# Kernel optimization log

Measured on AMD Instinct MI355X. Metric: run time of the kernel, lower is better.

The kernel has to match this reference:

```python
import jax, jax.numpy as jnp
import numpy as np

B, L, T = 8, 4096, 128
D_H, D_G, D_PROJ = 1024, 256, 256


def setup_inputs() -> dict:
    key = jax.random.key(0)
    k1, k2, k3, k4, k5 = jax.random.split(key, 5)
    H = jax.random.normal(k1, (B, L, D_H), dtype=jnp.float32)
    G = jax.random.normal(k2, (B, T, D_G), dtype=jnp.float32)
    mask = jax.random.randint(k3, (B, L), 0, 2) == 1  # True = masked out
    Wk = jax.random.normal(k4, (D_H, D_PROJ), dtype=jnp.float32) * 0.02
    Wq = jax.random.normal(k5, (D_G, D_PROJ), dtype=jnp.float32) * 0.02
    return {"H": H, "G": G, "mask": mask, "Wk": Wk, "Wq": Wq}


def reference(H, G, mask, Wk, Wq):
    scale = D_PROJ ** (-0.5)
    K = jnp.einsum('bld,dp->blp', H, Wk)          # [B, L, d_proj]
    Q = jnp.einsum('btd,dp->btp', G, Wq)          # [B, T, d_proj]
    logits = jnp.einsum('btp,blp->btl', Q, K) * scale  # [B, T, L]
    logits = jnp.where(mask[:, None, :], -jnp.inf, logits)
    alpha = jax.nn.softmax(logits, axis=-1)       # [B, T, L]
    Z = jnp.einsum('btl,bld->btd', alpha, H)      # [B, T, d_h]
    return Z
```

## Files before the change

kernel.cpp:

```cpp
#include <hip/hip_runtime.h>
#include <hip/hip_bf16.h>
#include <math.h>

#define B_  8
#define L_  4096
#define T_  128
#define DH  1024
#define DG  256
#define DP  256
#define BK  64
#define ZCH 8

typedef short bf16x8 __attribute__((ext_vector_type(8)));
typedef float f32x4  __attribute__((ext_vector_type(4)));
typedef unsigned short u16x8 __attribute__((ext_vector_type(8)));

#define AS1(p) ((const __attribute__((address_space(1))) void*)(p))
#define AS3(p) ((__attribute__((address_space(3))) void*)(p))

__device__ __forceinline__ unsigned short f2bf(float f) {
    unsigned u = __float_as_uint(f);
    unsigned r = (u + 0x7FFFu + ((u >> 16) & 1u)) >> 16;
    return (unsigned short)r;
}

__global__ __launch_bounds__(256) void wct_kernel(const float* __restrict__ Wk,
                                                  const float* __restrict__ Wq,
                                                  unsigned short* __restrict__ Wct) {
    __shared__ __attribute__((aligned(16))) unsigned short As[128 * BK];
    __shared__ __attribute__((aligned(16))) unsigned short Bs[64 * BK];
    const int n0 = blockIdx.x * 64, m0 = blockIdx.y * 128;
    const int tid = threadIdx.x, wave = tid >> 6, lane = tid & 63;
    const int lm = lane & 15, quad = lane >> 4;
    const int wm = wave >> 1, wn = wave & 1;
    const int bc = (tid & 15) * 4, br = tid >> 4;
    f32x4 acc[4][2] = {};

    for (int k0 = 0; k0 < DP; k0 += BK) {
        #pragma unroll
        for (int s = 0; s < 8; ++s) {
            const int row = br + s * 16;
            const float4 v = *(const float4*)(Wk + (size_t)(m0 + row) * DP + k0 + bc);
            ushort4 p; p.x = f2bf(v.x); p.y = f2bf(v.y); p.z = f2bf(v.z); p.w = f2bf(v.w);
            *(ushort4*)(&As[row * BK + bc]) = p;
        }
        #pragma unroll
        for (int s = 0; s < 4; ++s) {
            const int row = br + s * 16;
            const float4 v = *(const float4*)(Wq + (size_t)(n0 + row) * DP + k0 + bc);
            ushort4 p; p.x = f2bf(v.x); p.y = f2bf(v.y); p.z = f2bf(v.z); p.w = f2bf(v.w);
            *(ushort4*)(&Bs[row * BK + bc]) = p;
        }
        __syncthreads();
        #pragma unroll
        for (int ks = 0; ks < 2; ++ks) {
            bf16x8 a[4], bf[2];
            #pragma unroll
            for (int i = 0; i < 4; ++i)
                a[i] = *(const bf16x8*)(&As[(wm * 64 + i * 16 + lm) * BK + ks * 32 + quad * 8]);
            #pragma unroll
            for (int j = 0; j < 2; ++j)
                bf[j] = *(const bf16x8*)(&Bs[(wn * 32 + j * 16 + lm) * BK + ks * 32 + quad * 8]);
            #pragma unroll
            for (int i = 0; i < 4; ++i)
                #pragma unroll
                for (int j = 0; j < 2; ++j)
                    acc[i][j] = __builtin_amdgcn_mfma_f32_16x16x32_bf16(a[i], bf[j], acc[i][j], 0, 0, 0);
        }
        __syncthreads();
    }
    unsigned short* Cb = Wct + (size_t)m0 * DG + n0;
    #pragma unroll
    for (int i = 0; i < 4; ++i)
        #pragma unroll
        for (int j = 0; j < 2; ++j)
            #pragma unroll
            for (int r = 0; r < 4; ++r)
                Cb[(size_t)(wm * 64 + i * 16 + quad * 4 + r) * DG + wn * 32 + j * 16 + lm] =
                    f2bf(acc[i][j][r] * 0.0625f);
}

__global__ __launch_bounds__(256) void qproj_kernel(const float* __restrict__ G,
                                                    const unsigned short* __restrict__ Wct,
                                                    unsigned short* __restrict__ Qk) {
    __shared__ __attribute__((aligned(16))) unsigned short As[128 * BK];
    __shared__ __attribute__((aligned(16))) unsigned short Bs[64 * BK];
    const int n0 = blockIdx.x * 64, m0 = blockIdx.y * 128;
    const int tid = threadIdx.x, wave = tid >> 6, lane = tid & 63;
    const int lm = lane & 15, quad = lane >> 4;
    const int wm = wave >> 1, wn = wave & 1;
    const int bc = (tid & 15) * 4, br = tid >> 4;
    const int ar = lane >> 3, akb = (lane & 7) * 8;
    f32x4 acc[4][2] = {};

    for (int k0 = 0; k0 < DG; k0 += BK) {
        #pragma unroll
        for (int s = 0; s < 8; ++s) {
            const int row = br + s * 16;
            const float4 v = *(const float4*)(G + (size_t)(m0 + row) * DG + k0 + bc);
            ushort4 p; p.x = f2bf(v.x); p.y = f2bf(v.y); p.z = f2bf(v.z); p.w = f2bf(v.w);
            *(ushort4*)(&As[row * BK + bc]) = p;
        }
        #pragma unroll
        for (int s = 0; s < 2; ++s) {
            const int rowb = s * 32 + wave * 8;
            const unsigned short* gp = Wct + (size_t)(n0 + rowb + ar) * DG + k0 + akb;
            __builtin_amdgcn_global_load_lds(AS1(gp), AS3(&Bs[rowb * BK]), 16, 0, 0);
        }
        __syncthreads();
        #pragma unroll
        for (int ks = 0; ks < 2; ++ks) {
            bf16x8 a[4], bf[2];
            #pragma unroll
            for (int i = 0; i < 4; ++i)
                a[i] = *(const bf16x8*)(&As[(wm * 64 + i * 16 + lm) * BK + ks * 32 + quad * 8]);
            #pragma unroll
            for (int j = 0; j < 2; ++j)
                bf[j] = *(const bf16x8*)(&Bs[(wn * 32 + j * 16 + lm) * BK + ks * 32 + quad * 8]);
            #pragma unroll
            for (int i = 0; i < 4; ++i)
                #pragma unroll
                for (int j = 0; j < 2; ++j)
                    acc[i][j] = __builtin_amdgcn_mfma_f32_16x16x32_bf16(a[i], bf[j], acc[i][j], 0, 0, 0);
        }
        __syncthreads();
    }
    unsigned short* Cb = Qk + (size_t)m0 * DH + n0;
    #pragma unroll
    for (int i = 0; i < 4; ++i)
        #pragma unroll
        for (int j = 0; j < 2; ++j)
            #pragma unroll
            for (int r = 0; r < 4; ++r)
                Cb[(size_t)(wm * 64 + i * 16 + quad * 4 + r) * DH + wn * 32 + j * 16 + lm] =
                    f2bf(acc[i][j][r]);
}

__global__ __launch_bounds__(256, 2) void fusedsm_kernel(const unsigned short* __restrict__ Qk,
                                                         const float* __restrict__ H,
                                                         const int* __restrict__ mask,
                                                         unsigned short* __restrict__ alpha,
                                                         float* __restrict__ rowsum,
                                                         unsigned short* __restrict__ H16) {
    __shared__ __attribute__((aligned(16))) unsigned short As[T_ * BK];
    __shared__ __attribute__((aligned(16))) unsigned short Bs[64 * BK];
    __shared__ float rs[T_];
    const int blin = blockIdx.x + (L_ / 64) * blockIdx.y;
    const int b = blin & 7, l0 = (blin >> 3) * 64;
    const int tid = threadIdx.x, wave = tid >> 6, lane = tid & 63;
    const unsigned short* Ab = Qk + (size_t)b * T_ * DH;
    const float*          Hb = H + ((size_t)b * L_ + l0) * DH;
    unsigned short*     H16b = H16 + ((size_t)b * L_ + l0) * DH;

    const int lm = lane & 15, quad = lane >> 4;
    const int wm = wave >> 1, wn = wave & 1;
    f32x4 acc[4][2] = {};
    const int ar = lane >> 3, akb = (lane & 7) * 8;
    const int bc = (tid & 15) * 4, br = tid >> 4;

    if (tid < T_) rs[tid] = 0.f;

    for (int k0 = 0; k0 < DH; k0 += BK) {
        #pragma unroll
        for (int s = 0; s < 4; ++s) {
            const int rowb = s * 32 + wave * 8;
            const unsigned short* gp = Ab + (size_t)(rowb + ar) * DH + k0 + akb;
            __builtin_amdgcn_global_load_lds(AS1(gp), AS3(&As[rowb * BK]), 16, 0, 0);
        }
        #pragma unroll
        for (int s = 0; s < 4; ++s) {
            const int row = br + s * 16;
            const float4 v = *(const float4*)(Hb + (size_t)row * DH + k0 + bc);
            ushort4 pk; pk.x = f2bf(v.x); pk.y = f2bf(v.y); pk.z = f2bf(v.z); pk.w = f2bf(v.w);
            *(ushort4*)(&Bs[row * BK + bc]) = pk;
            *(ushort4*)(H16b + (size_t)row * DH + k0 + bc) = pk;
        }
        __syncthreads();
        #pragma unroll
        for (int ks = 0; ks < 2; ++ks) {
            bf16x8 a[4], bf[2];
            #pragma unroll
            for (int i = 0; i < 4; ++i)
                a[i] = *(const bf16x8*)(&As[(wm * 64 + i * 16 + lm) * BK + ks * 32 + quad * 8]);
            #pragma unroll
            for (int j = 0; j < 2; ++j)
                bf[j] = *(const bf16x8*)(&Bs[(wn * 32 + j * 16 + lm) * BK + ks * 32 + quad * 8]);
            #pragma unroll
            for (int i = 0; i < 4; ++i)
                #pragma unroll
                for (int j = 0; j < 2; ++j)
                    acc[i][j] = __builtin_amdgcn_mfma_f32_16x16x32_bf16(a[i], bf[j], acc[i][j], 0, 0, 0);
        }
        __syncthreads();
    }

    const int c0 = l0 + wn * 32 + lm;
    const int mk0 = mask[(size_t)b * L_ + c0];
    const int mk1 = mask[(size_t)b * L_ + c0 + 16];
    unsigned short* Arow = alpha + (size_t)b * T_ * L_ + l0 + wn * 32 + lm;
    #pragma unroll
    for (int i = 0; i < 4; ++i) {
        #pragma unroll
        for (int r = 0; r < 4; ++r) {
            const int row = wm * 64 + i * 16 + quad * 4 + r;
            float e0 = mk0 ? 0.f : __expf(acc[i][0][r]);
            float e1 = mk1 ? 0.f : __expf(acc[i][1][r]);
            Arow[(size_t)row * L_]      = f2bf(e0);
            Arow[(size_t)row * L_ + 16] = f2bf(e1);
            float part = e0 + e1;
            part += __shfl_xor(part, 1, 64);
            part += __shfl_xor(part, 2, 64);
            part += __shfl_xor(part, 4, 64);
            part += __shfl_xor(part, 8, 64);
            if (lm == 0) atomicAdd(&rs[row], part);
        }
    }
    __syncthreads();
    if (tid < T_) atomicAdd(&rowsum[(size_t)b * T_ + tid], rs[tid]);
}

__global__ __launch_bounds__(256, 2) void z_kernel(const unsigned short* __restrict__ alpha,
                                                   const unsigned short* __restrict__ H16,
                                                   const float* __restrict__ rowsum,
                                                   float* __restrict__ Z) {
    __shared__ __attribute__((aligned(16))) unsigned short As[T_ * BK];
    __shared__ __attribute__((aligned(16))) unsigned B32[128 * 32];
    const int blin = blockIdx.x + 8 * (blockIdx.y + 8 * blockIdx.z);
    const int ch = blin & 7, rest = blin >> 3;
    const int b = rest & 7, d0 = (rest >> 3) * 128;
    const int tid = threadIdx.x, wave = tid >> 6, lane = tid & 63;
    const int Lc = L_ / ZCH;
    const unsigned short* Ab = alpha + (size_t)b * T_ * L_ + ch * Lc;
    const unsigned short* Hb = H16 + ((size_t)b * L_ + ch * Lc) * DH + d0;

    const int lm = lane & 15, quad = lane >> 4;
    const int wm = wave >> 1, wn = wave & 1;
    f32x4 acc[4][4] = {};
    const int ar = lane >> 3, akb = (lane & 7) * 8;
    const int dg = tid & 15, lph = tid >> 4;

    for (int k0 = 0; k0 < Lc; k0 += BK) {
        #pragma unroll
        for (int s = 0; s < 4; ++s) {
            const int rowb = s * 32 + wave * 8;
            const unsigned short* gp = Ab + (size_t)(rowb + ar) * L_ + k0 + akb;
            __builtin_amdgcn_global_load_lds(AS1(gp), AS3(&As[rowb * BK]), 16, 0, 0);
        }
        {
            const unsigned short* r = Hb + (size_t)(k0 + 4 * lph) * DH + dg * 8;
            u16x8 u[4];
            #pragma unroll
            for (int rr = 0; rr < 4; ++rr)
                u[rr] = *(const u16x8*)(r + (size_t)rr * DH);
            const int lp0 = 2 * lph;
            #pragma unroll
            for (int i = 0; i < 8; ++i) {
                const int d   = dg * 8 + i;
                const int rot = ((i + (dg & 7)) << 2) & 31;
                B32[d * 32 + ((lp0 + rot) & 31)] =
                    (unsigned)u[0][i] | ((unsigned)u[1][i] << 16);
                B32[d * 32 + ((lp0 + 1 + rot) & 31)] =
                    (unsigned)u[2][i] | ((unsigned)u[3][i] << 16);
            }
        }
        __syncthreads();
        #pragma unroll
        for (int ks = 0; ks < 2; ++ks) {
            bf16x8 a[4], bf[4];
            #pragma unroll
            for (int i = 0; i < 4; ++i)
                a[i] = *(const bf16x8*)(&As[(wm * 64 + i * 16 + lm) * BK + ks * 32 + quad * 8]);
            #pragma unroll
            for (int j = 0; j < 4; ++j) {
                const int d   = wn * 64 + j * 16 + lm;
                const int rot = (((d & 7) + ((d >> 3) & 7)) << 2) & 31;
                bf[j] = *(const bf16x8*)(&B32[d * 32 + ((ks * 16 + quad * 4 + rot) & 31)]);
            }
            #pragma unroll
            for (int i = 0; i < 4; ++i)
                #pragma unroll
                for (int j = 0; j < 4; ++j)
                    acc[i][j] = __builtin_amdgcn_mfma_f32_16x16x32_bf16(a[i], bf[j], acc[i][j], 0, 0, 0);
        }
        __syncthreads();
    }
    float* Zb = Z + ((size_t)b * T_) * DH + d0;
    const float* rsb = rowsum + (size_t)b * T_;
    #pragma unroll
    for (int i = 0; i < 4; ++i) {
        #pragma unroll
        for (int r = 0; r < 4; ++r) {
            const int row = wm * 64 + i * 16 + quad * 4 + r;
            const float inv = 1.0f / rsb[row];
            #pragma unroll
            for (int j = 0; j < 4; ++j)
                atomicAdd(&Zb[(size_t)row * DH + wn * 64 + j * 16 + lm], acc[i][j][r] * inv);
        }
    }
}

extern "C" void kernel_launch(void* const* d_in, const int* in_sizes, int n_in,
                              void* d_out, int out_size, void* d_ws, size_t ws_size,
                              hipStream_t stream) {
    const float* H    = (const float*)d_in[0];
    const float* G    = (const float*)d_in[1];
    const int*   mask = (const int*)d_in[2];
    const float* Wk   = (const float*)d_in[3];
    const float* Wq   = (const float*)d_in[4];
    float* Z = (float*)d_out;

    char* ws = (char*)d_ws;
    unsigned short* Wct    = (unsigned short*)ws;
    unsigned short* Qk     = (unsigned short*)(ws + ((size_t)1 << 20));
    unsigned short* alpha  = (unsigned short*)(ws + ((size_t)4 << 20));
    float*          rowsum = (float*)(ws + ((size_t)13 << 20));
    unsigned short* H16    = (unsigned short*)(ws + ((size_t)14 << 20));

    hipMemsetAsync(rowsum, 0, (size_t)B_ * T_ * sizeof(float), stream);
    hipMemsetAsync(Z, 0, (size_t)B_ * T_ * DH * sizeof(float), stream);
    wct_kernel<<<dim3(DG / 64, DH / 128), 256, 0, stream>>>(Wk, Wq, Wct);
    qproj_kernel<<<dim3(DH / 64, (B_ * T_) / 128), 256, 0, stream>>>(G, Wct, Qk);
    fusedsm_kernel<<<dim3(L_ / 64, B_), 256, 0, stream>>>(Qk, H, mask, alpha, rowsum, H16);
    z_kernel<<<dim3(DH / 128, B_, ZCH), 256, 0, stream>>>(alpha, H16, rowsum, Z);
}
```

Baseline: 306.5 us.

## Double-buffer LDS in score and Z GEMMs; replace Z atomics with partial reduction

```diff
diff --git a/kernel.cpp b/kernel.cpp
--- a/kernel.cpp
+++ b/kernel.cpp
@@ -142,8 +142,8 @@
                                                          unsigned short* __restrict__ alpha,
                                                          float* __restrict__ rowsum,
                                                          unsigned short* __restrict__ H16) {
-    __shared__ __attribute__((aligned(16))) unsigned short As[T_ * BK];
-    __shared__ __attribute__((aligned(16))) unsigned short Bs[64 * BK];
+    __shared__ __attribute__((aligned(16))) unsigned short As[2][T_ * BK];
+    __shared__ __attribute__((aligned(16))) unsigned short Bs[2][64 * BK];
     __shared__ float rs[T_];
     const int blin = blockIdx.x + (L_ / 64) * blockIdx.y;
     const int b = blin & 7, l0 = (blin >> 3) * 64;
@@ -160,36 +160,66 @@
 
     if (tid < T_) rs[tid] = 0.f;
 
-    for (int k0 = 0; k0 < DH; k0 += BK) {
+    {
         #pragma unroll
         for (int s = 0; s < 4; ++s) {
             const int rowb = s * 32 + wave * 8;
-            const unsigned short* gp = Ab + (size_t)(rowb + ar) * DH + k0 + akb;
-            __builtin_amdgcn_global_load_lds(AS1(gp), AS3(&As[rowb * BK]), 16, 0, 0);
+            const unsigned short* gp = Ab + (size_t)(rowb + ar) * DH + akb;
+            __builtin_amdgcn_global_load_lds(AS1(gp), AS3(&As[0][rowb * BK]), 16, 0, 0);
         }
         #pragma unroll
         for (int s = 0; s < 4; ++s) {
             const int row = br + s * 16;
-            const float4 v = *(const float4*)(Hb + (size_t)row * DH + k0 + bc);
+            const float4 v = *(const float4*)(Hb + (size_t)row * DH + bc);
             ushort4 pk; pk.x = f2bf(v.x); pk.y = f2bf(v.y); pk.z = f2bf(v.z); pk.w = f2bf(v.w);
-            *(ushort4*)(&Bs[row * BK + bc]) = pk;
-            *(ushort4*)(H16b + (size_t)row * DH + k0 + bc) = pk;
-        }
-        __syncthreads();
+            *(ushort4*)(&Bs[0][row * BK + bc]) = pk;
+            *(ushort4*)(H16b + (size_t)row * DH + bc) = pk;
+        }
+    }
+    __syncthreads();
+
+    const int nT = DH / BK;
+    for (int t = 0; t < nT; ++t) {
+        const int p = t & 1, q = p ^ 1;
+        const int k1 = (t + 1) * BK;
+        float4 v[4];
+        if (t + 1 < nT) {
+            #pragma unroll
+            for (int s = 0; s < 4; ++s) {
+                const int rowb = s * 32 + wave * 8;
+                const unsigned short* gp = Ab + (size_t)(rowb + ar) * DH + k1 + akb;
+                __builtin_amdgcn_global_load_lds(AS1(gp), AS3(&As[q][rowb * BK]), 16, 0, 0);
+            }
+            #pragma unroll
+            for (int s = 0; s < 4; ++s) {
+                const int row = br + s * 16;
+                v[s] = *(const float4*)(Hb + (size_t)row * DH + k1 + bc);
+            }
+        }
         #pragma unroll
         for (int ks = 0; ks < 2; ++ks) {
             bf16x8 a[4], bf[2];
             #pragma unroll
             for (int i = 0; i < 4; ++i)
-                a[i] = *(const bf16x8*)(&As[(wm * 64 + i * 16 + lm) * BK + ks * 32 + quad * 8]);
+                a[i] = *(const bf16x8*)(&As[p][(wm * 64 + i * 16 + lm) * BK + ks * 32 + quad * 8]);
             #pragma unroll
             for (int j = 0; j < 2; ++j)
-                bf[j] = *(const bf16x8*)(&Bs[(wn * 32 + j * 16 + lm) * BK + ks * 32 + quad * 8]);
+                bf[j] = *(const bf16x8*)(&Bs[p][(wn * 32 + j * 16 + lm) * BK + ks * 32 + quad * 8]);
             #pragma unroll
             for (int i = 0; i < 4; ++i)
                 #pragma unroll
                 for (int j = 0; j < 2; ++j)
                     acc[i][j] = __builtin_amdgcn_mfma_f32_16x16x32_bf16(a[i], bf[j], acc[i][j], 0, 0, 0);
+        }
+        if (t + 1 < nT) {
+            #pragma unroll
+            for (int s = 0; s < 4; ++s) {
+                const int row = br + s * 16;
+                ushort4 pk; pk.x = f2bf(v[s].x); pk.y = f2bf(v[s].y);
+                pk.z = f2bf(v[s].z); pk.w = f2bf(v[s].w);
+                *(ushort4*)(&Bs[q][row * BK + bc]) = pk;
+                *(ushort4*)(H16b + (size_t)row * DH + k1 + bc) = pk;
+            }
         }
         __syncthreads();
     }
@@ -221,10 +251,9 @@
 
 __global__ __launch_bounds__(256, 2) void z_kernel(const unsigned short* __restrict__ alpha,
                                                    const unsigned short* __restrict__ H16,
-                                                   const float* __restrict__ rowsum,
-                                                   float* __restrict__ Z) {
-    __shared__ __attribute__((aligned(16))) unsigned short As[T_ * BK];
-    __shared__ __attribute__((aligned(16))) unsigned B32[128 * 32];
+                                                   float* __restrict__ part) {
+    __shared__ __attribute__((aligned(16))) unsigned short As[2][T_ * BK];
+    __shared__ __attribute__((aligned(16))) unsigned B32[2][128 * 32];
     const int blin = blockIdx.x + 8 * (blockIdx.y + 8 * blockIdx.z);
     const int ch = blin & 7, rest = blin >> 3;
     const int b = rest & 7, d0 = (rest >> 3) * 128;
@@ -238,65 +267,101 @@
     f32x4 acc[4][4] = {};
     const int ar = lane >> 3, akb = (lane & 7) * 8;
     const int dg = tid & 15, lph = tid >> 4;
-
-    for (int k0 = 0; k0 < Lc; k0 += BK) {
+    const int lp0 = 2 * lph;
+
+    {
         #pragma unroll
         for (int s = 0; s < 4; ++s) {
             const int rowb = s * 32 + wave * 8;
-            const unsigned short* gp = Ab + (size_t)(rowb + ar) * L_ + k0 + akb;
-            __builtin_amdgcn_global_load_lds(AS1(gp), AS3(&As[rowb * BK]), 16, 0, 0);
-        }
-        {
-            const unsigned short* r = Hb + (size_t)(k0 + 4 * lph) * DH + dg * 8;
-            u16x8 u[4];
+            const unsigned short* gp = Ab + (size_t)(rowb + ar) * L_ + akb;
+            __builtin_amdgcn_global_load_lds(AS1(gp), AS3(&As[0][rowb * BK]), 16, 0, 0);
+        }
+        const unsigned short* r = Hb + (size_t)(4 * lph) * DH + dg * 8;
+        u16x8 u[4];
+        #pragma unroll
+        for (int rr = 0; rr < 4; ++rr)
+            u[rr] = *(const u16x8*)(r + (size_t)rr * DH);
+        #pragma unroll
+        for (int i = 0; i < 8; ++i) {
+            const int d   = dg * 8 + i;
+            const int rot = ((i + (dg & 7)) << 2) & 31;
+            B32[0][d * 32 + ((lp0 + rot) & 31)]     = (unsigned)u[0][i] | ((unsigned)u[1][i] << 16);
+            B32[0][d * 32 + ((lp0 + 1 + rot) & 31)] = (unsigned)u[2][i] | ((unsigned)u[3][i] << 16);
+        }
+    }
+    __syncthreads();
+
+    const int nT = Lc / BK;
+    for (int t = 0; t < nT; ++t) {
+        const int p = t & 1, q = p ^ 1;
+        const int k1 = (t + 1) * BK;
+        u16x8 u[4];
+        if (t + 1 < nT) {
+            #pragma unroll
+            for (int s = 0; s < 4; ++s) {
+                const int rowb = s * 32 + wave * 8;
+                const unsigned short* gp = Ab + (size_t)(rowb + ar) * L_ + k1 + akb;
+                __builtin_amdgcn_global_load_lds(AS1(gp), AS3(&As[q][rowb * BK]), 16, 0, 0);
+            }
+            const unsigned short* r = Hb + (size_t)(k1 + 4 * lph) * DH + dg * 8;
             #pragma unroll
             for (int rr = 0; rr < 4; ++rr)
                 u[rr] = *(const u16x8*)(r + (size_t)rr * DH);
-            const int lp0 = 2 * lph;
+        }
+        #pragma unroll
+        for (int ks = 0; ks < 2; ++ks) {
+            bf16x8 a[4], bf[4];
+            #pragma unroll
+            for (int i = 0; i < 4; ++i)
+                a[i] = *(const bf16x8*)(&As[p][(wm * 64 + i * 16 + lm) * BK + ks * 32 + quad * 8]);
+            #pragma unroll
+            for (int j = 0; j < 4; ++j) {
+                const int d   = wn * 64 + j * 16 + lm;
+                const int rot = (((d & 7) + ((d >> 3) & 7)) << 2) & 31;
+                bf[j] = *(const bf16x8*)(&B32[p][d * 32 + ((ks * 16 + quad * 4 + rot) & 31)]);
+            }
+            #pragma unroll
+            for (int i = 0; i < 4; ++i)
+                #pragma unroll
+                for (int j = 0; j < 4; ++j)
+                    acc[i][j] = __builtin_amdgcn_mfma_f32_16x16x32_bf16(a[i], bf[j], acc[i][j], 0, 0, 0);
+        }
+        if (t + 1 < nT) {
             #pragma unroll
             for (int i = 0; i < 8; ++i) {
                 const int d   = dg * 8 + i;
                 const int rot = ((i + (dg & 7)) << 2) & 31;
-                B32[d * 32 + ((lp0 + rot) & 31)] =
-                    (unsigned)u[0][i] | ((unsigned)u[1][i] << 16);
-                B32[d * 32 + ((lp0 + 1 + rot) & 31)] =
-                    (unsigned)u[2][i] | ((unsigned)u[3][i] << 16);
-            }
-        }
-        __syncthreads();
-        #pragma unroll
-        for (int ks = 0; ks < 2; ++ks) {
-            bf16x8 a[4], bf[4];
-            #pragma unroll
-            for (int i = 0; i < 4; ++i)
-                a[i] = *(const bf16x8*)(&As[(wm * 64 + i * 16 + lm) * BK + ks * 32 + quad * 8]);
-            #pragma unroll
-            for (int j = 0; j < 4; ++j) {
-                const int d   = wn * 64 + j * 16 + lm;
-                const int rot = (((d & 7) + ((d >> 3) & 7)) << 2) & 31;
-                bf[j] = *(const bf16x8*)(&B32[d * 32 + ((ks * 16 + quad * 4 + rot) & 31)]);
-            }
-            #pragma unroll
-            for (int i = 0; i < 4; ++i)
-                #pragma unroll
-                for (int j = 0; j < 4; ++j)
-                    acc[i][j] = __builtin_amdgcn_mfma_f32_16x16x32_bf16(a[i], bf[j], acc[i][j], 0, 0, 0);
-        }
-        __syncthreads();
-    }
-    float* Zb = Z + ((size_t)b * T_) * DH + d0;
-    const float* rsb = rowsum + (size_t)b * T_;
-    #pragma unroll
-    for (int i = 0; i < 4; ++i) {
-        #pragma unroll
-        for (int r = 0; r < 4; ++r) {
-            const int row = wm * 64 + i * 16 + quad * 4 + r;
-            const float inv = 1.0f / rsb[row];
-            #pragma unroll
-            for (int j = 0; j < 4; ++j)
-                atomicAdd(&Zb[(size_t)row * DH + wn * 64 + j * 16 + lm], acc[i][j][r] * inv);
-        }
-    }
+                B32[q][d * 32 + ((lp0 + rot) & 31)]     = (unsigned)u[0][i] | ((unsigned)u[1][i] << 16);
+                B32[q][d * 32 + ((lp0 + 1 + rot) & 31)] = (unsigned)u[2][i] | ((unsigned)u[3][i] << 16);
+            }
+        }
+        __syncthreads();
+    }
+    float* Cb = part + (((size_t)ch * B_ + b) * T_) * DH + d0;
+    #pragma unroll
+    for (int i = 0; i < 4; ++i)
+        #pragma unroll
+        for (int j = 0; j < 4; ++j)
+            #pragma unroll
+            for (int r = 0; r < 4; ++r)
+                Cb[(size_t)(wm * 64 + i * 16 + quad * 4 + r) * DH + wn * 64 + j * 16 + lm] = acc[i][j][r];
+}
+
+__global__ __launch_bounds__(256) void zreduce_kernel(const float* __restrict__ p,
+                                                      const float* __restrict__ rowsum,
+                                                      float* __restrict__ Z) {
+    const size_t n = (size_t)B_ * T_ * DH;
+    const size_t i = ((size_t)blockIdx.x * 256 + threadIdx.x) * 4;
+    const int row = (int)(i >> 10);
+    const float inv = 1.0f / rowsum[row];
+    float4 o = {0.f, 0.f, 0.f, 0.f};
+    #pragma unroll
+    for (int c = 0; c < ZCH; ++c) {
+        const float4 a = *(const float4*)(p + (size_t)c * n + i);
+        o.x += a.x; o.y += a.y; o.z += a.z; o.w += a.w;
+    }
+    o.x *= inv; o.y *= inv; o.z *= inv; o.w *= inv;
+    *(float4*)(Z + i) = o;
 }
 
 extern "C" void kernel_launch(void* const* d_in, const int* in_sizes, int n_in,
@@ -315,11 +380,12 @@
     unsigned short* alpha  = (unsigned short*)(ws + ((size_t)4 << 20));
     float*          rowsum = (float*)(ws + ((size_t)13 << 20));
     unsigned short* H16    = (unsigned short*)(ws + ((size_t)14 << 20));
+    float*          zpart  = (float*)(ws + ((size_t)80 << 20));
 
     hipMemsetAsync(rowsum, 0, (size_t)B_ * T_ * sizeof(float), stream);
-    hipMemsetAsync(Z, 0, (size_t)B_ * T_ * DH * sizeof(float), stream);
     wct_kernel<<<dim3(DG / 64, DH / 128), 256, 0, stream>>>(Wk, Wq, Wct);
     qproj_kernel<<<dim3(DH / 64, (B_ * T_) / 128), 256, 0, stream>>>(G, Wct, Qk);
     fusedsm_kernel<<<dim3(L_ / 64, B_), 256, 0, stream>>>(Qk, H, mask, alpha, rowsum, H16);
-    z_kernel<<<dim3(DH / 128, B_, ZCH), 256, 0, stream>>>(alpha, H16, rowsum, Z);
-}
+    z_kernel<<<dim3(DH / 128, B_, ZCH), 256, 0, stream>>>(alpha, H16, zpart);
+    zreduce_kernel<<<(B_ * T_ * DH / 4) / 256, 256, 0, stream>>>(zpart, rowsum, Z);
+}
```

After: 286.3 us. -6.6%, faster.

## Double-buffer LDS with register prefetch and replace Z atomics with partial reduction

Applied to the files above, without the earlier changes.

```diff
diff --git a/kernel.cpp b/kernel.cpp
--- a/kernel.cpp
+++ b/kernel.cpp
@@ -18,10 +18,21 @@
 #define AS1(p) ((const __attribute__((address_space(1))) void*)(p))
 #define AS3(p) ((__attribute__((address_space(3))) void*)(p))
 
+#define SYNC() do { asm volatile("s_waitcnt lgkmcnt(0)" ::: "memory"); \
+                    __builtin_amdgcn_s_barrier(); \
+                    __builtin_amdgcn_sched_barrier(0); } while (0)
+
 __device__ __forceinline__ unsigned short f2bf(float f) {
     unsigned u = __float_as_uint(f);
     unsigned r = (u + 0x7FFFu + ((u >> 16) & 1u)) >> 16;
     return (unsigned short)r;
+}
+
+__device__ __forceinline__ char* swz(void* base, int row, int colbytes) {
+    return (char*)base + (((row << 7) + colbytes) ^ ((row & 7) << 4));
+}
+__device__ __forceinline__ const char* swzc(const void* base, int row, int colbytes) {
+    return (const char*)base + (((row << 7) + colbytes) ^ ((row & 7) << 4));
 }
 
 __global__ __launch_bounds__(256) void wct_kernel(const float* __restrict__ Wk,
@@ -142,8 +153,8 @@
                                                          unsigned short* __restrict__ alpha,
                                                          float* __restrict__ rowsum,
                                                          unsigned short* __restrict__ H16) {
-    __shared__ __attribute__((aligned(16))) unsigned short As[T_ * BK];
-    __shared__ __attribute__((aligned(16))) unsigned short Bs[64 * BK];
+    __shared__ __attribute__((aligned(16))) unsigned short As[2][T_ * BK];
+    __shared__ __attribute__((aligned(16))) unsigned short Bs[2][64 * BK];
     __shared__ float rs[T_];
     const int blin = blockIdx.x + (L_ / 64) * blockIdx.y;
     const int b = blin & 7, l0 = (blin >> 3) * 64;
@@ -160,38 +171,67 @@
 
     if (tid < T_) rs[tid] = 0.f;
 
-    for (int k0 = 0; k0 < DH; k0 += BK) {
-        #pragma unroll
-        for (int s = 0; s < 4; ++s) {
-            const int rowb = s * 32 + wave * 8;
-            const unsigned short* gp = Ab + (size_t)(rowb + ar) * DH + k0 + akb;
-            __builtin_amdgcn_global_load_lds(AS1(gp), AS3(&As[rowb * BK]), 16, 0, 0);
-        }
+    u16x8  qa0[4], qa1[4];
+    float4 hv0[4], hv1[4];
+
+    auto LOAD = [&](u16x8* qa, float4* hv, int kd) {
+        #pragma unroll
+        for (int s = 0; s < 4; ++s)
+            qa[s] = *(const u16x8*)(Ab + (size_t)(s * 32 + wave * 8 + ar) * DH + kd + akb);
+        #pragma unroll
+        for (int s = 0; s < 4; ++s)
+            hv[s] = *(const float4*)(Hb + (size_t)(br + s * 16) * DH + kd + bc);
+    };
+    auto WRITE = [&](int buf, const u16x8* qa, const float4* hv, int kd) {
+        #pragma unroll
+        for (int s = 0; s < 4; ++s)
+            *(u16x8*)swz(&As[buf][0], s * 32 + wave * 8 + ar, akb * 2) = qa[s];
         #pragma unroll
         for (int s = 0; s < 4; ++s) {
             const int row = br + s * 16;
-            const float4 v = *(const float4*)(Hb + (size_t)row * DH + k0 + bc);
-            ushort4 pk; pk.x = f2bf(v.x); pk.y = f2bf(v.y); pk.z = f2bf(v.z); pk.w = f2bf(v.w);
-            *(ushort4*)(&Bs[row * BK + bc]) = pk;
-            *(ushort4*)(H16b + (size_t)row * DH + k0 + bc) = pk;
-        }
-        __syncthreads();
+            ushort4 pk; pk.x = f2bf(hv[s].x); pk.y = f2bf(hv[s].y);
+            pk.z = f2bf(hv[s].z); pk.w = f2bf(hv[s].w);
+            *(ushort4*)swz(&Bs[buf][0], row, bc * 2) = pk;
+            *(ushort4*)(H16b + (size_t)row * DH + kd + bc) = pk;
+        }
+    };
+    auto COMPUTE = [&](int buf) {
         #pragma unroll
         for (int ks = 0; ks < 2; ++ks) {
-            bf16x8 a[4], bf[2];
-            #pragma unroll
-            for (int i = 0; i < 4; ++i)
-                a[i] = *(const bf16x8*)(&As[(wm * 64 + i * 16 + lm) * BK + ks * 32 + quad * 8]);
-            #pragma unroll
-            for (int j = 0; j < 2; ++j)
-                bf[j] = *(const bf16x8*)(&Bs[(wn * 32 + j * 16 + lm) * BK + ks * 32 + quad * 8]);
+            bf16x8 a[4], bfv[2];
+            #pragma unroll
+            for (int i = 0; i < 4; ++i) {
+                const int row = wm * 64 + i * 16 + lm;
+                a[i] = *(const bf16x8*)swzc(&As[buf][0], row, ks * 64 + quad * 16);
+            }
+            #pragma unroll
+            for (int j = 0; j < 2; ++j) {
+                const int row = wn * 32 + j * 16 + lm;
+                bfv[j] = *(const bf16x8*)swzc(&Bs[buf][0], row, ks * 64 + quad * 16);
+            }
             #pragma unroll
             for (int i = 0; i < 4; ++i)
                 #pragma unroll
                 for (int j = 0; j < 2; ++j)
-                    acc[i][j] = __builtin_amdgcn_mfma_f32_16x16x32_bf16(a[i], bf[j], acc[i][j], 0, 0, 0);
-        }
-        __syncthreads();
+                    acc[i][j] = __builtin_amdgcn_mfma_f32_16x16x32_bf16(a[i], bfv[j], acc[i][j], 0, 0, 0);
+        }
+    };
+
+    const int nT = DH / BK;
+    LOAD(qa0, hv0, 0);
+    LOAD(qa1, hv1, BK);
+    WRITE(0, qa0, hv0, 0);
+    SYNC();
+
+    for (int tt = 0; tt < nT; tt += 2) {
+        if (tt + 2 < nT) LOAD(qa0, hv0, (tt + 2) * BK);
+        COMPUTE(0);
+        WRITE(1, qa1, hv1, (tt + 1) * BK);
+        SYNC();
+        if (tt + 3 < nT) LOAD(qa1, hv1, (tt + 3) * BK);
+        COMPUTE(1);
+        if (tt + 2 < nT) WRITE(0, qa0, hv0, (tt + 2) * BK);
+        SYNC();
     }
 
     const int c0 = l0 + wn * 32 + lm;
@@ -221,10 +261,9 @@
 
 __global__ __launch_bounds__(256, 2) void z_kernel(const unsigned short* __restrict__ alpha,
                                                    const unsigned short* __restrict__ H16,
-                                                   const float* __restrict__ rowsum,
-                                                   float* __restrict__ Z) {
-    __shared__ __attribute__((aligned(16))) unsigned short As[T_ * BK];
-    __shared__ __attribute__((aligned(16))) unsigned B32[128 * 32];
+                                                   float* __restrict__ part) {
+    __shared__ __attribute__((aligned(16))) unsigned short As[2][T_ * BK];
+    __shared__ __attribute__((aligned(16))) unsigned B32[2][128 * 32];
     const int blin = blockIdx.x + 8 * (blockIdx.y + 8 * blockIdx.z);
     const int ch = blin & 7, rest = blin >> 3;
     const int b = rest & 7, d0 = (rest >> 3) * 128;
@@ -238,65 +277,97 @@
     f32x4 acc[4][4] = {};
     const int ar = lane >> 3, akb = (lane & 7) * 8;
     const int dg = tid & 15, lph = tid >> 4;
-
-    for (int k0 = 0; k0 < Lc; k0 += BK) {
-        #pragma unroll
-        for (int s = 0; s < 4; ++s) {
-            const int rowb = s * 32 + wave * 8;
-            const unsigned short* gp = Ab + (size_t)(rowb + ar) * L_ + k0 + akb;
-            __builtin_amdgcn_global_load_lds(AS1(gp), AS3(&As[rowb * BK]), 16, 0, 0);
-        }
-        {
-            const unsigned short* r = Hb + (size_t)(k0 + 4 * lph) * DH + dg * 8;
-            u16x8 u[4];
-            #pragma unroll
-            for (int rr = 0; rr < 4; ++rr)
-                u[rr] = *(const u16x8*)(r + (size_t)rr * DH);
-            const int lp0 = 2 * lph;
-            #pragma unroll
-            for (int i = 0; i < 8; ++i) {
-                const int d   = dg * 8 + i;
-                const int rot = ((i + (dg & 7)) << 2) & 31;
-                B32[d * 32 + ((lp0 + rot) & 31)] =
-                    (unsigned)u[0][i] | ((unsigned)u[1][i] << 16);
-                B32[d * 32 + ((lp0 + 1 + rot) & 31)] =
-                    (unsigned)u[2][i] | ((unsigned)u[3][i] << 16);
+    const int lp0 = 2 * lph;
+
+    u16x8 qa0[4], qa1[4];
+    u16x8 hu0[4], hu1[4];
+
+    auto LOAD = [&](u16x8* qa, u16x8* hu, int kd) {
+        #pragma unroll
+        for (int s = 0; s < 4; ++s)
+            qa[s] = *(const u16x8*)(Ab + (size_t)(s * 32 + wave * 8 + ar) * L_ + kd + akb);
+        const unsigned short* r = Hb + (size_t)(kd + 4 * lph) * DH + dg * 8;
+        #pragma unroll
+        for (int rr = 0; rr < 4; ++rr)
+            hu[rr] = *(const u16x8*)(r + (size_t)rr * DH);
+    };
+    auto WRITE = [&](int buf, const u16x8* qa, const u16x8* hu) {
+        #pragma unroll
+        for (int s = 0; s < 4; ++s)
+            *(u16x8*)swz(&As[buf][0], s * 32 + wave * 8 + ar, akb * 2) = qa[s];
+        #pragma unroll
+        for (int i = 0; i < 8; ++i) {
+            const int d   = dg * 8 + i;
+            const int rot = ((i + (dg & 7)) << 2) & 31;
+            B32[buf][d * 32 + ((lp0 + rot) & 31)]     = (unsigned)hu[0][i] | ((unsigned)hu[1][i] << 16);
+            B32[buf][d * 32 + ((lp0 + 1 + rot) & 31)] = (unsigned)hu[2][i] | ((unsigned)hu[3][i] << 16);
+        }
+    };
+    auto COMPUTE = [&](int buf) {
+        #pragma unroll
+        for (int ks = 0; ks < 2; ++ks) {
+            bf16x8 a[4], bfv[4];
+            #pragma unroll
+            for (int i = 0; i < 4; ++i) {
+                const int row = wm * 64 + i * 16 + lm;
+                a[i] = *(const bf16x8*)swzc(&As[buf][0], row, ks * 64 + quad * 16);
             }
-        }
-        __syncthreads();
-        #pragma unroll
-        for (int ks = 0; ks < 2; ++ks) {
-            bf16x8 a[4], bf[4];
-            #pragma unroll
-            for (int i = 0; i < 4; ++i)
-                a[i] = *(const bf16x8*)(&As[(wm * 64 + i * 16 + lm) * BK + ks * 32 + quad * 8]);
             #pragma unroll
             for (int j = 0; j < 4; ++j) {
                 const int d   = wn * 64 + j * 16 + lm;
                 const int rot = (((d & 7) + ((d >> 3) & 7)) << 2) & 31;
-                bf[j] = *(const bf16x8*)(&B32[d * 32 + ((ks * 16 + quad * 4 + rot) & 31)]);
+                bfv[j] = *(const bf16x8*)(&B32[buf][d * 32 + ((ks * 16 + quad * 4 + rot) & 31)]);
             }
             #pragma unroll
             for (int i = 0; i < 4; ++i)
                 #pragma unroll
                 for (int j = 0; j < 4; ++j)
-                    acc[i][j] = __builtin_amdgcn_mfma_f32_16x16x32_bf16(a[i], bf[j], acc[i][j], 0, 0, 0);
-        }
-        __syncthreads();
-    }
-    float* Zb = Z + ((size_t)b * T_) * DH + d0;
-    const float* rsb = rowsum + (size_t)b * T_;
-    #pragma unroll
-    for (int i = 0; i < 4; ++i) {
-        #pragma unroll
-        for (int r = 0; r < 4; ++r) {
-            const int row = wm * 64 + i * 16 + quad * 4 + r;
-            const float inv = 1.0f / rsb[row];
-            #pragma unroll
-            for (int j = 0; j < 4; ++j)
-                atomicAdd(&Zb[(size_t)row * DH + wn * 64 + j * 16 + lm], acc[i][j][r] * inv);
-        }
-    }
+                    acc[i][j] = __builtin_amdgcn_mfma_f32_16x16x32_bf16(a[i], bfv[j], acc[i][j], 0, 0, 0);
+        }
+    };
+
+    const int nT = Lc / BK;
+    LOAD(qa0, hu0, 0);
+    LOAD(qa1, hu1, BK);
+    WRITE(0, qa0, hu0);
+    SYNC();
+
+    for (int tt = 0; tt < nT; tt += 2) {
+        if (tt + 2 < nT) LOAD(qa0, hu0, (tt + 2) * BK);
+        COMPUTE(0);
+        WRITE(1, qa1, hu1);
+        SYNC();
+        if (tt + 3 < nT) LOAD(qa1, hu1, (tt + 3) * BK);
+        COMPUTE(1);
+        if (tt + 2 < nT) WRITE(0, qa0, hu0);
+        SYNC();
+    }
+
+    float* Cb = part + (((size_t)ch * B_ + b) * T_) * DH + d0;
+    #pragma unroll
+    for (int i = 0; i < 4; ++i)
+        #pragma unroll
+        for (int j = 0; j < 4; ++j)
+            #pragma unroll
+            for (int r = 0; r < 4; ++r)
+                Cb[(size_t)(wm * 64 + i * 16 + quad * 4 + r) * DH + wn * 64 + j * 16 + lm] = acc[i][j][r];
+}
+
+__global__ __launch_bounds__(256) void zreduce_kernel(const float* __restrict__ p,
+                                                      const float* __restrict__ rowsum,
+                                                      float* __restrict__ Z) {
+    const size_t n = (size_t)B_ * T_ * DH;
+    const size_t i = ((size_t)blockIdx.x * 256 + threadIdx.x) * 4;
+    const int row = (int)(i >> 10);
+    const float inv = 1.0f / rowsum[row];
+    float4 o = {0.f, 0.f, 0.f, 0.f};
+    #pragma unroll
+    for (int c = 0; c < ZCH; ++c) {
+        const float4 a = *(const float4*)(p + (size_t)c * n + i);
+        o.x += a.x; o.y += a.y; o.z += a.z; o.w += a.w;
+    }
+    o.x *= inv; o.y *= inv; o.z *= inv; o.w *= inv;
+    *(float4*)(Z + i) = o;
 }
 
 extern "C" void kernel_launch(void* const* d_in, const int* in_sizes, int n_in,
@@ -315,11 +386,12 @@
     unsigned short* alpha  = (unsigned short*)(ws + ((size_t)4 << 20));
     float*          rowsum = (float*)(ws + ((size_t)13 << 20));
     unsigned short* H16    = (unsigned short*)(ws + ((size_t)14 << 20));
+    float*          zpart  = (float*)(ws + ((size_t)80 << 20));
 
     hipMemsetAsync(rowsum, 0, (size_t)B_ * T_ * sizeof(float), stream);
-    hipMemsetAsync(Z, 0, (size_t)B_ * T_ * DH * sizeof(float), stream);
     wct_kernel<<<dim3(DG / 64, DH / 128), 256, 0, stream>>>(Wk, Wq, Wct);
     qproj_kernel<<<dim3(DH / 64, (B_ * T_) / 128), 256, 0, stream>>>(G, Wct, Qk);
     fusedsm_kernel<<<dim3(L_ / 64, B_), 256, 0, stream>>>(Qk, H, mask, alpha, rowsum, H16);
-    z_kernel<<<dim3(DH / 128, B_, ZCH), 256, 0, stream>>>(alpha, H16, rowsum, Z);
-}
+    z_kernel<<<dim3(DH / 128, B_, ZCH), 256, 0, stream>>>(alpha, H16, zpart);
+    zreduce_kernel<<<(B_ * T_ * DH / 4) / 256, 256, 0, stream>>>(zpart, rowsum, Z);
+}
```

Result: faster. 282.9 us (-7.7%).
